# Kernel optimization log

Hardware: AMD Instinct MI355X
Metric: run time of the kernel (lower is better)

## Reference

```python
import jax, jax.numpy as jnp
import numpy as np

N = 50000      # nodes
E = 800000     # edges
T = 3          # npass
ED = 64        # embedding_dim
NS = 23        # nshifts (arange(0.8, 3.0+1e-5, 0.1))
MD = NS + ED   # message_dim = 87
H = 200        # hidden width (hardcoded in module)
NMOL = 2048    # number of molecules (segments for final scatter)
RD = ED * (T + 1)  # readout input dim = 256
EPS = 1e-5

SHIFTS = jnp.asarray(np.arange(0.8, 3.0 + 1e-5, 0.1, dtype=np.float32))  # [23]


def setup_inputs() -> dict:
    key = jax.random.key(0)
    ks = jax.random.split(key, 32)
    inp = {
        'z_i': jax.random.randint(ks[0], (N,), 0, 10),
        'edge_index': jax.random.randint(ks[1], (2, E), 0, N),
        'dist_ij': jax.random.uniform(ks[2], (E, 1), dtype=jnp.float32) * 2.2 + 0.8,
        'mol_ind': jnp.sort(jax.random.randint(ks[3], (N,), 0, NMOL)),
        'emb': jax.random.normal(ks[4], (10, ED), dtype=jnp.float32),
        # per-pass update MLP params, stacked over T
        'up_bn_g': jnp.ones((T, MD), jnp.float32),
        'up_bn_b': jnp.zeros((T, MD), jnp.float32),
        'up_w1': jax.random.normal(ks[5], (T, MD, H), jnp.float32) * 0.05,
        'up_b1': jnp.zeros((T, H), jnp.float32),
        'up_w2': jax.random.normal(ks[6], (T, H, H), jnp.float32) * 0.05,
        'up_b2': jnp.zeros((T, H), jnp.float32),
        'up_w3': jax.random.normal(ks[7], (T, H, H), jnp.float32) * 0.05,
        'up_b3': jnp.zeros((T, H), jnp.float32),
        'up_w4': jax.random.normal(ks[8], (T, H, ED), jnp.float32) * 0.05,
        'up_b4': jnp.zeros((T, ED), jnp.float32),
        # readout MLP params
        'ro_bn_g': jnp.ones((RD,), jnp.float32),
        'ro_bn_b': jnp.zeros((RD,), jnp.float32),
        'ro_w1': jax.random.normal(ks[9], (RD, H), jnp.float32) * 0.05,
        'ro_b1': jnp.zeros((H,), jnp.float32),
        'ro_w2': jax.random.normal(ks[10], (H, H), jnp.float32) * 0.05,
        'ro_b2': jnp.zeros((H,), jnp.float32),
        'ro_w3': jax.random.normal(ks[11], (H, H), jnp.float32) * 0.05,
        'ro_b3': jnp.zeros((H,), jnp.float32),
        'ro_w4': jax.random.normal(ks[12], (H, 1), jnp.float32) * 0.05,
        'ro_b4': jnp.zeros((1,), jnp.float32),  # bias filled to 0 in __init__
    }
    return inp


def batchnorm(x, g, b):
    # BatchNorm1d in training mode: batch statistics, biased variance
    mu = jnp.mean(x, axis=0)
    var = jnp.mean(jnp.square(x - mu), axis=0)
    return (x - mu) * jax.lax.rsqrt(var + EPS) * g + b


def mlp(x, g, b, w1, b1, w2, b2, w3, b3, w4, b4):
    x = batchnorm(x, g, b)
    x = jax.nn.relu(x @ w1 + b1)
    x = jax.nn.relu(x @ w2 + b2)
    x = jax.nn.relu(x @ w3 + b3)
    return x @ w4 + b4


def reference(z_i, edge_index, dist_ij, mol_ind, emb,
              up_bn_g, up_bn_b, up_w1, up_b1, up_w2, up_b2, up_w3, up_b3, up_w4, up_b4,
              ro_bn_g, ro_bn_b, ro_w1, ro_b1, ro_w2, ro_b2, ro_w3, ro_b3, ro_w4, ro_b4):
    e_source, e_sink = edge_index[0], edge_index[1]
    rbf_ij = jnp.exp(-jnp.square(dist_ij - SHIFTS[None, :]))  # [E, NS]
    x_i = emb[z_i]                                            # [N, ED]
    x_list = [x_i]
    for t in range(T):
        m_ij = jnp.concatenate([rbf_ij, x_i[e_sink]], axis=1)  # [E, MD] gather
        m_i = jax.ops.segment_sum(m_ij, e_source, num_segments=N)  # scatter-sum
        x_i = x_i + 0.1 * mlp(m_i, up_bn_g[t], up_bn_b[t],
                              up_w1[t], up_b1[t], up_w2[t], up_b2[t],
                              up_w3[t], up_b3[t], up_w4[t], up_b4[t])
        x_list.append(x_i)
    x_all = jnp.concatenate(x_list, axis=1)  # [N, RD]
    y_i = mlp(x_all, ro_bn_g, ro_bn_b, ro_w1, ro_b1, ro_w2, ro_b2, ro_w3, ro_b3, ro_w4, ro_b4)
    y = jax.ops.segment_sum(y_i, mol_ind, num_segments=NMOL)  # [NMOL, 1]
    return y
```

## Files before the change

### kernel.cpp

```cpp
#include <hip/hip_runtime.h>
#include <hip/hip_bf16.h>
#include <type_traits>

#define NN 50000
#define NP 50048
#define EE 800000
#define TT 3
#define ED 64
#define NS 23
#define MD 87
#define HH 200
#define NMOL 2048
#define RD 256

#define SW 232
#define NPB2 512
#define SNB ((NN + 255) / 256)

typedef __attribute__((ext_vector_type(8))) short short8b;
typedef __attribute__((ext_vector_type(4))) float f32x4;

template <int V> using ic = std::integral_constant<int, V>;

__device__ __forceinline__ unsigned short f2bf(float f) {
  unsigned u = __float_as_uint(f);
  return (unsigned short)((u + 0x7fffu + ((u >> 16) & 1u)) >> 16);
}
__device__ __forceinline__ float ubf2f(unsigned short h) {
  return __uint_as_float(((unsigned)h) << 16);
}
__device__ __forceinline__ float bfp2f(unsigned p) {
  return __uint_as_float(p << 16) + __uint_as_float(p & 0xffff0000u);
}
__device__ __forceinline__ unsigned packsplit(float v) {
  unsigned short h = f2bf(v);
  unsigned short l = f2bf(v - ubf2f(h));
  return (unsigned)h | ((unsigned)l << 16);
}

struct WD { const float* src; short* dst; int K, N, Kpad, Npad, T; };
struct WDs { WD d[5]; };

__global__ __launch_bounds__(256) void wprep_kernel(WDs W) {
  WD w = W.d[blockIdx.y];
  int KB = w.Kpad >> 5, NT = w.Npad >> 4;
  int per = w.Npad * w.Kpad;
  int total = w.T * per;
  for (int idx = blockIdx.x * 256 + threadIdx.x; idx < total; idx += gridDim.x * 256) {
    int t = idx / per;
    int r = idx - t * per;
    int e = r & 7, lane = (r >> 3) & 63;
    int blk = r >> 9;
    int kb = blk % KB, tile = blk / KB;
    int ln = lane & 15, quad = lane >> 4;
    int n = tile * 16 + ln, k = kb * 32 + quad * 8 + e;
    float v = 0.f;
    if (k < w.K && n < w.N) v = w.src[((size_t)t * w.K + k) * w.N + n];
    unsigned short h = f2bf(v);
    unsigned short l = f2bf(v - ubf2f(h));
    size_t base = ((size_t)(t * NT + tile) * KB + kb) * 1024;
    w.dst[base + lane * 8 + e] = (short)h;
    w.dst[base + 512 + lane * 8 + e] = (short)l;
  }
}

__global__ __launch_bounds__(256) void wscale_kernel(const float* __restrict__ wsrc,
                                                     const float* __restrict__ na,
                                                     const float* __restrict__ nb,
                                                     const float* __restrict__ bsrc,
                                                     int K, int Kpad,
                                                     short* __restrict__ wsp,
                                                     float* __restrict__ bc) {
  int n = blockIdx.x;
  int k = threadIdx.x;
  int KB = Kpad >> 5;
  int tile = n >> 4, ln = n & 15;
  float contrib = 0.f;
  if (k < Kpad) {
    float v = 0.f;
    if (n < HH && k < K) {
      float w = wsrc[(size_t)k * HH + n];
      v = na[k] * w;
      contrib = nb[k] * w;
    }
    unsigned short h = f2bf(v);
    unsigned short l = f2bf(v - ubf2f(h));
    int kb = k >> 5, quad = (k & 31) >> 3, e = k & 7;
    int lane = quad * 16 + ln;
    size_t base = ((size_t)tile * KB + kb) * 1024;
    wsp[base + lane * 8 + e] = (short)h;
    wsp[base + 512 + lane * 8 + e] = (short)l;
  }
  __shared__ float sh[256];
  sh[k] = contrib;
  __syncthreads();
  for (int off = 128; off > 0; off >>= 1) {
    if (k < off) sh[k] += sh[k + off];
    __syncthreads();
  }
  if (k == 0) bc[n] = (n < HH ? bsrc[n] : 0.f) + sh[0];
}

__global__ __launch_bounds__(256) void emb_kernel(const int* __restrict__ z,
                                                  const float* __restrict__ emb,
                                                  unsigned* __restrict__ xp,
                                                  short* __restrict__ xq,
                                                  short* __restrict__ xqs) {
  int idx = blockIdx.x * 256 + threadIdx.x;
  if (idx >= NN * ED) return;
  int i = idx >> 6, d = idx & 63;
  unsigned pk = packsplit(emb[z[i] * ED + d]);
  xp[(size_t)i * RD + d] = pk;
  short h = (short)(pk & 0xffffu);
  xq[(size_t)i * RD + d] = h;
  xqs[(size_t)i * ED + d] = h;
}

__global__ __launch_bounds__(256) void hist_kernel(const int* __restrict__ src,
                                                   int* __restrict__ deg) {
  int e = blockIdx.x * 256 + threadIdx.x;
  if (e < EE) atomicAdd(&deg[src[e]], 1);
}

__global__ __launch_bounds__(256) void scanA_kernel(const int* __restrict__ deg,
                                                    int* __restrict__ Psum) {
  int i = blockIdx.x * 256 + threadIdx.x;
  int v = (i < NN) ? deg[i] : 0;
#pragma unroll
  for (int off = 32; off > 0; off >>= 1) v += __shfl_down(v, off, 64);
  __shared__ int ws[4];
  if ((threadIdx.x & 63) == 0) ws[threadIdx.x >> 6] = v;
  __syncthreads();
  if (threadIdx.x == 0) Psum[blockIdx.x] = ws[0] + ws[1] + ws[2] + ws[3];
}

__global__ __launch_bounds__(256) void scanB_kernel(const int* __restrict__ Psum,
                                                    int* __restrict__ Poff) {
  __shared__ int sh[256];
  int t = threadIdx.x;
  int v = (t < SNB) ? Psum[t] : 0;
  sh[t] = v;
  __syncthreads();
  for (int off = 1; off < 256; off <<= 1) {
    int u = (t >= off) ? sh[t - off] : 0;
    __syncthreads();
    sh[t] += u;
    __syncthreads();
  }
  if (t < SNB) Poff[t] = sh[t] - v;
}

__global__ __launch_bounds__(256) void scanC_kernel(const int* __restrict__ deg,
                                                    const int* __restrict__ Poff,
                                                    int* __restrict__ offs,
                                                    int* __restrict__ cursor) {
  __shared__ int sh[256];
  int t = threadIdx.x;
  int i = blockIdx.x * 256 + t;
  int v = (i < NN) ? deg[i] : 0;
  sh[t] = v;
  __syncthreads();
  for (int off = 1; off < 256; off <<= 1) {
    int u = (t >= off) ? sh[t - off] : 0;
    __syncthreads();
    sh[t] += u;
    __syncthreads();
  }
  int excl = Poff[blockIdx.x] + sh[t] - v;
  if (i < NN) {
    offs[i] = excl;
    cursor[i] = excl;
    if (i == NN - 1) offs[NN] = excl + v;
  }
}

__global__ __launch_bounds__(256) void scatter_kernel(const int* __restrict__ src,
                                                      const int* __restrict__ snk,
                                                      const float* __restrict__ dist,
                                                      int* __restrict__ cursor,
                                                      int* __restrict__ ssink,
                                                      float* __restrict__ sdist) {
  int e = blockIdx.x * 256 + threadIdx.x;
  if (e >= EE) return;
  int p = atomicAdd(&cursor[src[e]], 1);
  ssink[p] = snk[e];
  sdist[p] = dist[e];
}

template <bool RBF>
__global__ __launch_bounds__(256) void gather_kernel(const int* __restrict__ offs,
                                                     const int* __restrict__ ssink,
                                                     const float* __restrict__ sdist,
                                                     const short* __restrict__ xqs,
                                                     short* __restrict__ mh) {
  int node = blockIdx.x * 4 + (threadIdx.x >> 6);
  int lane = threadIdx.x & 63;
  if (node >= NN) return;
  float shift = (float)(0.8 + 0.1 * (double)lane);
  int e0 = offs[node], e1 = offs[node + 1];
  float ax0 = 0.f, ax1 = 0.f, ar0 = 0.f, ar1 = 0.f;
  int j = e0;
  for (; j + 4 <= e1; j += 4) {
    int s0 = ssink[j], s1 = ssink[j + 1], s2 = ssink[j + 2], s3 = ssink[j + 3];
    float x0 = ubf2f((unsigned short)xqs[(size_t)s0 * ED + lane]);
    float x1 = ubf2f((unsigned short)xqs[(size_t)s1 * ED + lane]);
    float x2 = ubf2f((unsigned short)xqs[(size_t)s2 * ED + lane]);
    float x3 = ubf2f((unsigned short)xqs[(size_t)s3 * ED + lane]);
    ax0 += x0 + x2;
    ax1 += x1 + x3;
    if (RBF && lane < NS) {
      float d0 = sdist[j], d1 = sdist[j + 1], d2 = sdist[j + 2], d3 = sdist[j + 3];
      float u0 = d0 - shift, u1 = d1 - shift, u2 = d2 - shift, u3 = d3 - shift;
      ar0 += __expf(-u0 * u0) + __expf(-u2 * u2);
      ar1 += __expf(-u1 * u1) + __expf(-u3 * u3);
    }
  }
  for (; j < e1; j++) {
    int s = ssink[j];
    ax0 += ubf2f((unsigned short)xqs[(size_t)s * ED + lane]);
    if (RBF && lane < NS) {
      float u = sdist[j] - shift;
      ar0 += __expf(-u * u);
    }
  }
  float accx = ax0 + ax1;
  if (RBF && lane < NS) mh[(size_t)node * 96 + lane] = (short)f2bf(ar0 + ar1);
  if (RBF && lane >= NS && lane < 32) mh[(size_t)node * 96 + 64 + lane] = 0;
  mh[(size_t)node * 96 + NS + lane] = (short)f2bf(accx);
}

template <int LD>
__global__ __launch_bounds__(256) void colstats_s16_kernel(const short* __restrict__ X,
                                                           float* __restrict__ P) {
  constexpr int CG = LD / 8;
  constexpr int RPB = 256 / CG;
  const int t = threadIdx.x;
  const int cg = t % CG, rin = t / CG;
  float s[8] = {0, 0, 0, 0, 0, 0, 0, 0}, q[8] = {0, 0, 0, 0, 0, 0, 0, 0};
  if (rin < RPB) {
    for (int r = blockIdx.x * RPB + rin; r < NN; r += gridDim.x * RPB) {
      union { uint4 v; short e[8]; } u;
      u.v = *(const uint4*)(X + (size_t)r * LD + cg * 8);
#pragma unroll
      for (int e = 0; e < 8; e++) {
        float f = ubf2f((unsigned short)u.e[e]);
        s[e] += f;
        q[e] += f * f;
      }
    }
  }
  __shared__ float sh[256][16];
#pragma unroll
  for (int e = 0; e < 8; e++) { sh[t][e] = s[e]; sh[t][8 + e] = q[e]; }
  __syncthreads();
  if (rin == 0) {
    for (int rr = 1; rr < RPB; rr++) {
      const float* o = sh[rr * CG + cg];
#pragma unroll
      for (int e = 0; e < 8; e++) { s[e] += o[e]; q[e] += o[8 + e]; }
    }
    float* Pb = P + blockIdx.x * 512;
#pragma unroll
    for (int e = 0; e < 8; e++) {
      Pb[cg * 8 + e] = s[e];
      Pb[256 + cg * 8 + e] = q[e];
    }
  }
}

__global__ __launch_bounds__(256) void bnfinal2_kernel(const float* __restrict__ P, int nblk,
                                                       const float* __restrict__ g,
                                                       const float* __restrict__ b, int ncols,
                                                       float* __restrict__ na,
                                                       float* __restrict__ nb) {
  int c = blockIdx.x;
  int t = threadIdx.x;
  float s = 0.f, q = 0.f;
  for (int i = t; i < nblk; i += 256) {
    s += P[i * 512 + c];
    q += P[i * 512 + 256 + c];
  }
#pragma unroll
  for (int off = 32; off > 0; off >>= 1) {
    s += __shfl_down(s, off, 64);
    q += __shfl_down(q, off, 64);
  }
  __shared__ float ws[4], wq[4];
  if ((t & 63) == 0) { ws[t >> 6] = s; wq[t >> 6] = q; }
  __syncthreads();
  if (t == 0) {
    s = ws[0] + ws[1] + ws[2] + ws[3];
    q = wq[0] + wq[1] + wq[2] + wq[3];
    if (c < ncols) {
      float mean = s / (float)NN;
      float var = q / (float)NN - mean * mean;
      float a = g[c] * rsqrtf(var + 1e-5f);
      na[c] = a;
      nb[c] = b[c] - mean * a;
    } else {
      na[c] = 0.f;
      nb[c] = 0.f;
    }
  }
}

template <bool READOUT>
__global__ __launch_bounds__(64, 3) void fused_kernel(
    const short* __restrict__ Agh,
    const short* __restrict__ W1p, const short* __restrict__ W2p,
    const short* __restrict__ W3p, const short* __restrict__ W4p,
    const float* __restrict__ b1, const float* __restrict__ b2,
    const float* __restrict__ b3, const float* __restrict__ b4,
    unsigned* __restrict__ xp, short* __restrict__ xq, short* __restrict__ xqs,
    int t, const float* __restrict__ w4ro, const int* __restrict__ mol,
    float* __restrict__ out) {
  __shared__ short ldsW[16 * SW];
  constexpr int GLDA = READOUT ? RD : 96;
  constexpr int KB1 = READOUT ? 8 : 3;
  const int lane = threadIdx.x;
  const int ln = lane & 15, quad = lane >> 4, q8 = quad * 8;
  const int bm = blockIdx.x * 16;
  const short* aRow = ldsW + ln * SW;

#pragma unroll
  for (int p = 0; p < 6; p++) {
    int idx = p * 64 + lane;
    ldsW[(idx / 24) * SW + 208 + (idx % 24)] = 0;
  }

  f32x4 acc[7];
  short8b a[7];

  auto mat = [&](auto ntt, auto kbt, auto tt, const short8b* af,
                 const short* __restrict__ Wp, int j0) {
    constexpr int NT = decltype(ntt)::value;
    constexpr int KB = decltype(kbt)::value;
    constexpr int TERMS = decltype(tt)::value;
#pragma unroll
    for (int j = 0; j < NT; j++) acc[j] = (f32x4){0.f, 0.f, 0.f, 0.f};
#pragma unroll
    for (int kb = 0; kb < KB; kb++) {
      short8b bh[NT];
#pragma unroll
      for (int j = 0; j < NT; j++)
        bh[j] = *(const short8b*)(Wp + (size_t)((j0 + j) * KB + kb) * 1024 + lane * 8);
#pragma unroll
      for (int j = 0; j < NT; j++)
        acc[j] = __builtin_amdgcn_mfma_f32_16x16x32_bf16(af[kb], bh[j], acc[j], 0, 0, 0);
    }
    if constexpr (TERMS == 2) {
#pragma unroll
      for (int kb = 0; kb < KB; kb++) {
        short8b bl[NT];
#pragma unroll
        for (int j = 0; j < NT; j++)
          bl[j] = *(const short8b*)(Wp + (size_t)((j0 + j) * KB + kb) * 1024 + 512 + lane * 8);
#pragma unroll
        for (int j = 0; j < NT; j++)
          acc[j] = __builtin_amdgcn_mfma_f32_16x16x32_bf16(af[kb], bl[j], acc[j], 0, 0, 0);
      }
    }
  };
  auto epi = [&](auto ntt, int j0, const float* __restrict__ bias) {
    constexpr int NT = decltype(ntt)::value;
#pragma unroll
    for (int j = 0; j < NT; j++) {
      int colg = (j0 + j) * 16 + ln;
      float bb = (colg < HH) ? bias[colg] : 0.f;
#pragma unroll
      for (int r = 0; r < 4; r++)
        ldsW[(quad * 4 + r) * SW + colg] = (short)f2bf(fmaxf(acc[j][r] + bb, 0.f));
    }
  };
  auto loadA = [&]() {
#pragma unroll
    for (int kb = 0; kb < 7; kb++)
      a[kb] = *(const short8b*)(aRow + kb * 32 + q8);
  };

  {
    short8b a1[KB1];
#pragma unroll
    for (int kb = 0; kb < KB1; kb++)
      a1[kb] = *(const short8b*)(Agh + (size_t)(bm + ln) * GLDA + kb * 32 + q8);
    mat(ic<7>{}, ic<KB1>{}, ic<2>{}, a1, W1p, 0);
    epi(ic<7>{}, 0, b1);
    mat(ic<6>{}, ic<KB1>{}, ic<2>{}, a1, W1p, 7);
    epi(ic<6>{}, 7, b1);
  }

  loadA();
  mat(ic<7>{}, ic<7>{}, ic<1>{}, a, W2p, 0);
  epi(ic<7>{}, 0, b2);
  mat(ic<6>{}, ic<7>{}, ic<1>{}, a, W2p, 7);
  epi(ic<6>{}, 7, b2);

  loadA();
  mat(ic<7>{}, ic<7>{}, ic<1>{}, a, W3p, 0);
  epi(ic<7>{}, 0, b3);
  mat(ic<6>{}, ic<7>{}, ic<1>{}, a, W3p, 7);
  epi(ic<6>{}, 7, b3);

  loadA();

  if constexpr (!READOUT) {
    mat(ic<4>{}, ic<7>{}, ic<2>{}, a, W4p, 0);
#pragma unroll
    for (int j = 0; j < 4; j++) {
      int colg = j * 16 + ln;
      float bb = b4[colg];
#pragma unroll
      for (int r = 0; r < 4; r++) {
        int grow = bm + quad * 4 + r;
        if (grow < NN) {
          size_t base = (size_t)grow * RD;
          float oldv = bfp2f(xp[base + (size_t)t * ED + colg]);
          unsigned pk = packsplit(oldv + 0.1f * (acc[j][r] + bb));
          xp[base + (size_t)(t + 1) * ED + colg] = pk;
          short h = (short)(pk & 0xffffu);
          xq[base + (size_t)(t + 1) * ED + colg] = h;
          xqs[(size_t)(t + 1) * NN * ED + (size_t)grow * ED + colg] = h;
        }
      }
    }
  } else {
    float s = 0.f;
#pragma unroll
    for (int kb = 0; kb < 7; kb++)
      if (kb * 32 + q8 < HH)
#pragma unroll
        for (int e = 0; e < 8; e++)
          s += ubf2f((unsigned short)a[kb][e]) * w4ro[kb * 32 + q8 + e];
    s += __shfl_xor(s, 16, 64);
    s += __shfl_xor(s, 32, 64);
    int grow = bm + ln;
    if (lane < 16 && grow < NN) atomicAdd(&out[mol[grow]], s + b4[0]);
  }
}

extern "C" void kernel_launch(void* const* d_in, const int* in_sizes, int n_in,
                              void* d_out, int out_size, void* d_ws, size_t ws_size,
                              hipStream_t stream) {
  const int* z_i = (const int*)d_in[0];
  const int* e_src = (const int*)d_in[1];
  const int* e_snk = ((const int*)d_in[1]) + EE;
  const float* dist = (const float*)d_in[2];
  const int* mol = (const int*)d_in[3];
  const float* emb = (const float*)d_in[4];
  const float* up_bn_g = (const float*)d_in[5];
  const float* up_bn_b = (const float*)d_in[6];
  const float* up_w1 = (const float*)d_in[7];
  const float* up_b1 = (const float*)d_in[8];
  const float* up_w2 = (const float*)d_in[9];
  const float* up_b2 = (const float*)d_in[10];
  const float* up_w3 = (const float*)d_in[11];
  const float* up_b3 = (const float*)d_in[12];
  const float* up_w4 = (const float*)d_in[13];
  const float* up_b4 = (const float*)d_in[14];
  const float* ro_bn_g = (const float*)d_in[15];
  const float* ro_bn_b = (const float*)d_in[16];
  const float* ro_w1 = (const float*)d_in[17];
  const float* ro_b1 = (const float*)d_in[18];
  const float* ro_w2 = (const float*)d_in[19];
  const float* ro_b2 = (const float*)d_in[20];
  const float* ro_w3 = (const float*)d_in[21];
  const float* ro_b3 = (const float*)d_in[22];
  const float* ro_w4 = (const float*)d_in[23];
  const float* ro_b4 = (const float*)d_in[24];
  float* out = (float*)d_out;

  char* p = (char*)d_ws;
  auto alloc = [&](size_t bytes) {
    void* r = (void*)p;
    p += (bytes + 255) & ~(size_t)255;
    return r;
  };
  unsigned* x_p = (unsigned*)alloc((size_t)NN * RD * 4);
  short* x_q = (short*)alloc((size_t)NP * RD * 2);
  short* x_qs = (short*)alloc((size_t)(TT + 1) * NN * ED * 2);
  short* mh = (short*)alloc((size_t)NP * 96 * 2);
  int* ssink = (int*)alloc((size_t)EE * 4);
  float* sdist = (float*)alloc((size_t)EE * 4);
  int* offs = (int*)alloc((size_t)(NN + 1) * 4);
  int* deg = (int*)alloc((size_t)NN * 4);
  int* cursor = (int*)alloc((size_t)NN * 4);
  int* Psum = (int*)alloc((size_t)SNB * 4);
  int* Poff = (int*)alloc((size_t)SNB * 4);
  float* P = (float*)alloc((size_t)NPB2 * 512 * 4);
  float* na = (float*)alloc(256 * 4);
  float* nb = (float*)alloc(256 * 4);
  float* b1c = (float*)alloc(208 * 4);
  short* w1sp = (short*)alloc((size_t)13 * 3 * 1024 * 2);
  short* r1sp = (short*)alloc((size_t)13 * 8 * 1024 * 2);
  short* w2p = (short*)alloc((size_t)TT * 13 * 7 * 1024 * 2);
  short* w3p = (short*)alloc((size_t)TT * 13 * 7 * 1024 * 2);
  short* w4p = (short*)alloc((size_t)TT * 4 * 7 * 1024 * 2);
  short* r2p = (short*)alloc((size_t)13 * 7 * 1024 * 2);
  short* r3p = (short*)alloc((size_t)13 * 7 * 1024 * 2);

  hipMemsetAsync(deg, 0, (size_t)NN * 4, stream);
  hipMemsetAsync(out, 0, (size_t)NMOL * 4, stream);

  WDs descs;
  descs.d[0] = {up_w2, w2p, HH, HH, 224, 208, TT};
  descs.d[1] = {up_w3, w3p, HH, HH, 224, 208, TT};
  descs.d[2] = {up_w4, w4p, HH, ED, 224, 64, TT};
  descs.d[3] = {ro_w2, r2p, HH, HH, 224, 208, 1};
  descs.d[4] = {ro_w3, r3p, HH, HH, 224, 208, 1};
  wprep_kernel<<<dim3(546, 5), 256, 0, stream>>>(descs);

  emb_kernel<<<(NN * ED + 255) / 256, 256, 0, stream>>>(z_i, emb, x_p, x_q, x_qs);
  hist_kernel<<<(EE + 255) / 256, 256, 0, stream>>>(e_src, deg);
  scanA_kernel<<<SNB, 256, 0, stream>>>(deg, Psum);
  scanB_kernel<<<1, 256, 0, stream>>>(Psum, Poff);
  scanC_kernel<<<SNB, 256, 0, stream>>>(deg, Poff, offs, cursor);
  scatter_kernel<<<(EE + 255) / 256, 256, 0, stream>>>(e_src, e_snk, dist, cursor, ssink, sdist);

  const int gM = NP / 16;

  for (int t = 0; t < TT; t++) {
    if (t == 0)
      gather_kernel<true><<<(NN + 3) / 4, 256, 0, stream>>>(
          offs, ssink, sdist, x_qs, mh);
    else
      gather_kernel<false><<<(NN + 3) / 4, 256, 0, stream>>>(
          offs, ssink, sdist, x_qs + (size_t)t * NN * ED, mh);
    colstats_s16_kernel<96><<<NPB2, 256, 0, stream>>>(mh, P);
    bnfinal2_kernel<<<256, 256, 0, stream>>>(P, NPB2, up_bn_g + t * MD, up_bn_b + t * MD, MD,
                                             na, nb);
    wscale_kernel<<<208, 256, 0, stream>>>(up_w1 + (size_t)t * MD * HH, na, nb,
                                           up_b1 + t * HH, MD, 96, w1sp, b1c);
    fused_kernel<false><<<gM, 64, 0, stream>>>(
        mh, w1sp,
        w2p + (size_t)t * 13 * 7 * 1024, w3p + (size_t)t * 13 * 7 * 1024,
        w4p + (size_t)t * 4 * 7 * 1024,
        b1c, up_b2 + t * HH, up_b3 + t * HH, up_b4 + t * ED,
        x_p, x_q, x_qs, t, nullptr, nullptr, nullptr);
  }

  colstats_s16_kernel<256><<<NPB2, 256, 0, stream>>>(x_q, P);
  bnfinal2_kernel<<<256, 256, 0, stream>>>(P, NPB2, ro_bn_g, ro_bn_b, RD, na, nb);
  wscale_kernel<<<208, 256, 0, stream>>>(ro_w1, na, nb, ro_b1, RD, 256, r1sp, b1c);
  fused_kernel<true><<<gM, 64, 0, stream>>>(
      x_q, r1sp, r2p, r3p, nullptr,
      b1c, ro_b2, ro_b3, ro_b4,
      nullptr, nullptr, nullptr, 0, ro_w4, mol, out);

  (void)in_sizes; (void)n_in; (void)out_size; (void)ws_size;
}
```

Baseline: 631.0 us.

## Share MLP weight tiles across four waves via double-buffered LDS staging

```diff
diff --git a/kernel.cpp b/kernel.cpp
--- a/kernel.cpp
+++ b/kernel.cpp
@@ -36,6 +36,12 @@
   unsigned short h = f2bf(v);
   unsigned short l = f2bf(v - ubf2f(h));
   return (unsigned)h | ((unsigned)l << 16);
+}
+
+__device__ __forceinline__ void gl2lds16(const short* g, short* l) {
+  __builtin_amdgcn_global_load_lds(
+      (const __attribute__((address_space(1))) unsigned int*)g,
+      (__attribute__((address_space(3))) unsigned int*)l, 16, 0, 0);
 }
 
 struct WD { const float* src; short* dst; int K, N, Kpad, Npad, T; };
@@ -305,7 +311,7 @@
 }
 
 template <bool READOUT>
-__global__ __launch_bounds__(64, 3) void fused_kernel(
+__global__ __launch_bounds__(256, 2) void fused_kernel(
     const short* __restrict__ Agh,
     const short* __restrict__ W1p, const short* __restrict__ W2p,
     const short* __restrict__ W3p, const short* __restrict__ W4p,
@@ -314,12 +320,15 @@
     unsigned* __restrict__ xp, short* __restrict__ xq, short* __restrict__ xqs,
     int t, const float* __restrict__ w4ro, const int* __restrict__ mol,
     float* __restrict__ out) {
-  __shared__ short ldsW[16 * SW];
+  __shared__ short ldsA[4 * 16 * SW];
+  __shared__ short ldsB[2][13 * 512];
   constexpr int GLDA = READOUT ? RD : 96;
   constexpr int KB1 = READOUT ? 8 : 3;
-  const int lane = threadIdx.x;
-  const int ln = lane & 15, quad = lane >> 4, q8 = quad * 8;
-  const int bm = blockIdx.x * 16;
+  const int tid = threadIdx.x;
+  const int wave = tid >> 6, lane = tid & 63, ln = lane & 15, quad = lane >> 4;
+  const int q8 = quad * 8;
+  const int bm = blockIdx.x * 64 + wave * 16;
+  short* ldsW = ldsA + wave * (16 * SW);
   const short* aRow = ldsW + ln * SW;
 
 #pragma unroll
@@ -328,44 +337,49 @@
     ldsW[(idx / 24) * SW + 208 + (idx % 24)] = 0;
   }
 
-  f32x4 acc[7];
+  f32x4 acc[13];
   short8b a[7];
 
-  auto mat = [&](auto ntt, auto kbt, auto tt, const short8b* af,
-                 const short* __restrict__ Wp, int j0) {
+  auto stage = [&](auto ntt, auto kbt, const short* __restrict__ Wp, int s, int buf) {
+    constexpr int NT = decltype(ntt)::value;
+    constexpr int KB = decltype(kbt)::value;
+    const int kb = (s < KB) ? s : s - KB;
+    const int plane = (s < KB) ? 0 : 512;
+    for (int tile = wave; tile < NT; tile += 4)
+      gl2lds16(Wp + (size_t)(tile * KB + kb) * 1024 + plane + lane * 8,
+               ldsB[buf] + tile * 512);
+  };
+
+  auto runlayer = [&](auto ntt, auto kbt, auto tt, const short8b* af,
+                      const short* __restrict__ Wp) {
     constexpr int NT = decltype(ntt)::value;
     constexpr int KB = decltype(kbt)::value;
     constexpr int TERMS = decltype(tt)::value;
+    constexpr int NSL = KB * TERMS;
 #pragma unroll
     for (int j = 0; j < NT; j++) acc[j] = (f32x4){0.f, 0.f, 0.f, 0.f};
-#pragma unroll
-    for (int kb = 0; kb < KB; kb++) {
+    stage(ntt, kbt, Wp, 0, 0);
+    __syncthreads();
+#pragma unroll
+    for (int s = 0; s < NSL; s++) {
+      if (s + 1 < NSL) stage(ntt, kbt, Wp, s + 1, (s + 1) & 1);
+      const int kb = (s < KB) ? s : s - KB;
       short8b bh[NT];
 #pragma unroll
       for (int j = 0; j < NT; j++)
-        bh[j] = *(const short8b*)(Wp + (size_t)((j0 + j) * KB + kb) * 1024 + lane * 8);
+        bh[j] = *(const short8b*)(ldsB[s & 1] + j * 512 + lane * 8);
 #pragma unroll
       for (int j = 0; j < NT; j++)
         acc[j] = __builtin_amdgcn_mfma_f32_16x16x32_bf16(af[kb], bh[j], acc[j], 0, 0, 0);
-    }
-    if constexpr (TERMS == 2) {
-#pragma unroll
-      for (int kb = 0; kb < KB; kb++) {
-        short8b bl[NT];
-#pragma unroll
-        for (int j = 0; j < NT; j++)
-          bl[j] = *(const short8b*)(Wp + (size_t)((j0 + j) * KB + kb) * 1024 + 512 + lane * 8);
-#pragma unroll
-        for (int j = 0; j < NT; j++)
-          acc[j] = __builtin_amdgcn_mfma_f32_16x16x32_bf16(af[kb], bl[j], acc[j], 0, 0, 0);
-      }
+      __syncthreads();
     }
   };
-  auto epi = [&](auto ntt, int j0, const float* __restrict__ bias) {
+
+  auto epi = [&](auto ntt, const float* __restrict__ bias) {
     constexpr int NT = decltype(ntt)::value;
 #pragma unroll
     for (int j = 0; j < NT; j++) {
-      int colg = (j0 + j) * 16 + ln;
+      int colg = j * 16 + ln;
       float bb = (colg < HH) ? bias[colg] : 0.f;
 #pragma unroll
       for (int r = 0; r < 4; r++)
@@ -383,28 +397,22 @@
 #pragma unroll
     for (int kb = 0; kb < KB1; kb++)
       a1[kb] = *(const short8b*)(Agh + (size_t)(bm + ln) * GLDA + kb * 32 + q8);
-    mat(ic<7>{}, ic<KB1>{}, ic<2>{}, a1, W1p, 0);
-    epi(ic<7>{}, 0, b1);
-    mat(ic<6>{}, ic<KB1>{}, ic<2>{}, a1, W1p, 7);
-    epi(ic<6>{}, 7, b1);
+    runlayer(ic<13>{}, ic<KB1>{}, ic<2>{}, a1, W1p);
+    epi(ic<13>{}, b1);
   }
 
   loadA();
-  mat(ic<7>{}, ic<7>{}, ic<1>{}, a, W2p, 0);
-  epi(ic<7>{}, 0, b2);
-  mat(ic<6>{}, ic<7>{}, ic<1>{}, a, W2p, 7);
-  epi(ic<6>{}, 7, b2);
+  runlayer(ic<13>{}, ic<7>{}, ic<1>{}, a, W2p);
+  epi(ic<13>{}, b2);
 
   loadA();
-  mat(ic<7>{}, ic<7>{}, ic<1>{}, a, W3p, 0);
-  epi(ic<7>{}, 0, b3);
-  mat(ic<6>{}, ic<7>{}, ic<1>{}, a, W3p, 7);
-  epi(ic<6>{}, 7, b3);
+  runlayer(ic<13>{}, ic<7>{}, ic<1>{}, a, W3p);
+  epi(ic<13>{}, b3);
 
   loadA();
 
   if constexpr (!READOUT) {
-    mat(ic<4>{}, ic<7>{}, ic<2>{}, a, W4p, 0);
+    runlayer(ic<4>{}, ic<7>{}, ic<2>{}, a, W4p);
 #pragma unroll
     for (int j = 0; j < 4; j++) {
       int colg = j * 16 + ln;
@@ -516,7 +524,7 @@
   scanC_kernel<<<SNB, 256, 0, stream>>>(deg, Poff, offs, cursor);
   scatter_kernel<<<(EE + 255) / 256, 256, 0, stream>>>(e_src, e_snk, dist, cursor, ssink, sdist);
 
-  const int gM = NP / 16;
+  const int gM = NP / 64;
 
   for (int t = 0; t < TT; t++) {
     if (t == 0)
@@ -530,7 +538,7 @@
                                              na, nb);
     wscale_kernel<<<208, 256, 0, stream>>>(up_w1 + (size_t)t * MD * HH, na, nb,
                                            up_b1 + t * HH, MD, 96, w1sp, b1c);
-    fused_kernel<false><<<gM, 64, 0, stream>>>(
+    fused_kernel<false><<<gM, 256, 0, stream>>>(
         mh, w1sp,
         w2p + (size_t)t * 13 * 7 * 1024, w3p + (size_t)t * 13 * 7 * 1024,
         w4p + (size_t)t * 4 * 7 * 1024,
@@ -541,7 +549,7 @@
   colstats_s16_kernel<256><<<NPB2, 256, 0, stream>>>(x_q, P);
   bnfinal2_kernel<<<256, 256, 0, stream>>>(P, NPB2, ro_bn_g, ro_bn_b, RD, na, nb);
   wscale_kernel<<<208, 256, 0, stream>>>(ro_w1, na, nb, ro_b1, RD, 256, r1sp, b1c);
-  fused_kernel<true><<<gM, 64, 0, stream>>>(
+  fused_kernel<true><<<gM, 256, 0, stream>>>(
       x_q, r1sp, r2p, r3p, nullptr,
       b1c, ro_b2, ro_b3, ro_b4,
       nullptr, nullptr, nullptr, 0, ro_w4, mol, out);
```

New measurement: 622.6 us. No clear change (-1.3%).
